# Kernel optimization log

Hardware: AMD Instinct MI355X
Metric: run time of the kernel (lower is better)

Reference implementation:

```python
import jax, jax.numpy as jnp
import numpy as np

B, CDD, HIS, S, D, NH, FF, V, K = 8, 5, 50, 64, 768, 12, 3072, 30522, 8


def _ln(x):
    mu = x.mean(-1, keepdims=True)
    var = ((x - mu) ** 2).mean(-1, keepdims=True)
    return (x - mu) / jnp.sqrt(var + 1e-12)


def _transformer(x, mask, Wq, Wk, Wv, Wo, W1, W2):
    # x: [..., S, D]; mask: [..., S] (float, >0 means valid)
    lead = x.shape[:-2]
    s, d = x.shape[-2], x.shape[-1]
    dh = d // NH
    x2 = x.reshape(-1, s, d)
    m = mask.reshape(-1, s)
    split = lambda t: t.reshape(-1, s, NH, dh).transpose(0, 2, 1, 3)
    q, k, v = split(x2 @ Wq), split(x2 @ Wk), split(x2 @ Wv)
    logits = jnp.einsum('nhqd,nhkd->nhqk', q, k) / jnp.sqrt(jnp.float32(dh))
    logits = logits + jnp.where(m > 0, 0.0, -1e9)[:, None, None, :]
    a = jax.nn.softmax(logits, axis=-1)
    o = jnp.einsum('nhqk,nhkd->nhqd', a, v).transpose(0, 2, 1, 3).reshape(-1, s, d) @ Wo
    h = _ln(x2 + o)
    h = _ln(h + jax.nn.gelu(h @ W1) @ W2)
    h = h.reshape(*lead, s, d)
    return h, h[..., 0, :]


def _build_prefix(subword_index, mask):
    # subword_index: [B, n, S, 2] int; mask: [B, n, 1] float
    b, n = subword_index.shape[0], subword_index.shape[1]
    flat = subword_index[..., 0] * S + subword_index[..., 1]  # [B, n, S]
    dest = jnp.zeros((b * n, S * S), jnp.float32)
    dest = dest.at[jnp.arange(b * n)[:, None], flat.reshape(b * n, S)].set(1.0)
    dest = dest * mask.reshape(b * n, 1)
    prefix = dest.reshape(b, n, S, S)
    # granularity == 'avg' -> L1 normalize rows
    prefix = prefix / jnp.maximum(prefix.sum(-1, keepdims=True), 1e-12)
    return prefix


def setup_inputs() -> dict:
    key = jax.random.key(0)
    ks = jax.random.split(key, 24)
    w = lambda k, shp: jax.random.normal(k, shp, jnp.float32) * 0.02
    inp = {
        'cdd_subword_index': jax.random.randint(ks[0], (B, CDD, S, 2), 0, S, jnp.int32),
        'his_subword_index': jax.random.randint(ks[1], (B, HIS, S, 2), 0, S, jnp.int32),
        'cdd_encoded_index': jax.random.randint(ks[2], (B, CDD, S), 0, V, jnp.int32),
        'his_encoded_index': jax.random.randint(ks[3], (B, HIS, S), 0, V, jnp.int32),
        'cdd_mask': jnp.ones((B, CDD, 1), jnp.float32),
        'his_mask': jnp.ones((B, HIS, 1), jnp.float32),
        'cdd_attn_mask': jnp.ones((B, CDD, S), jnp.float32),
        'his_attn_mask': jnp.ones((B, HIS, S), jnp.float32),
        'emb': w(ks[4], (V, D)),
        'bert_Wq': w(ks[5], (D, D)), 'bert_Wk': w(ks[6], (D, D)),
        'bert_Wv': w(ks[7], (D, D)), 'bert_Wo': w(ks[8], (D, D)),
        'bert_W1': w(ks[9], (D, FF)), 'bert_W2': w(ks[10], (FF, D)),
        'encN_Wq': w(ks[11], (D, D)), 'encN_Wk': w(ks[12], (D, D)),
        'encN_Wv': w(ks[13], (D, D)), 'encN_Wo': w(ks[14], (D, D)),
        'encN_W1': w(ks[15], (D, FF)), 'encN_W2': w(ks[16], (FF, D)),
        'qU': w(ks[17], (D,)),
        'proj_W': w(ks[18], (D, D)), 'proj_b': jnp.zeros((D,), jnp.float32),
    }
    return inp


def reference(cdd_subword_index, his_subword_index, cdd_encoded_index, his_encoded_index,
              cdd_mask, his_mask, cdd_attn_mask, his_attn_mask, emb,
              bert_Wq, bert_Wk, bert_Wv, bert_Wo, bert_W1, bert_W2,
              encN_Wq, encN_Wk, encN_Wv, encN_Wo, encN_W1, encN_W2,
              qU, proj_W, proj_b):
    rt_d = jnp.sqrt(jnp.float32(D))
    # scatter-built one-hot subword->token prefix matrices
    cdd_prefix = _build_prefix(cdd_subword_index, cdd_mask)   # [B,C,S,S]
    his_prefix = _build_prefix(his_subword_index, his_mask)   # [B,H,S,S]
    # pooled attention masks: prefix @ mask
    cdd_attn = jnp.einsum('bcst,bct->bcs', cdd_prefix, cdd_attn_mask)
    his_attn = jnp.einsum('bnst,bnt->bns', his_prefix, his_attn_mask)
    # embedding lookup + subword->token pooling
    cdd_emb = jnp.einsum('bcst,bctd->bcsd', cdd_prefix, emb[cdd_encoded_index])
    his_emb = jnp.einsum('bnst,bntd->bnsd', his_prefix, emb[his_encoded_index])
    # candidate news: BERT encode, take CLS, project
    _, cdd_cls = _transformer(cdd_emb, cdd_attn, bert_Wq, bert_Wk, bert_Wv, bert_Wo, bert_W1, bert_W2)
    cdd_repr = jnp.tanh(cdd_cls @ proj_W + proj_b)            # [B,C,D]
    # history news encoder
    his_hidden, his_cls = _transformer(his_emb, his_attn, encN_Wq, encN_Wk, encN_Wv, encN_Wo, encN_W1, encN_W2)
    # user encoder: attention pooling over history news reprs
    wgt = jax.nn.softmax(jnp.einsum('bnd,d->bn', his_cls, qU) / rt_d, axis=-1)
    user0 = jnp.einsum('bn,bnd->bd', wgt, his_cls)            # [B,D]
    # matching reducer: top-k personalized terms per history news
    scores = jnp.einsum('bnsd,bd->bns', his_hidden, user0) / rt_d
    scores = jnp.where(his_attn > 0, scores, -1e9)
    _, kid = jax.lax.top_k(scores, K)                         # [B,H,K]
    ps_terms = jnp.take_along_axis(his_hidden, kid[..., None], axis=2).reshape(B, HIS * K, D)
    ps_mask = jnp.take_along_axis(his_attn, kid, axis=2).reshape(B, HIS * K)
    # user BERT over selected terms
    _, user_cls = _transformer(ps_terms, ps_mask, bert_Wq, bert_Wk, bert_Wv, bert_Wo, bert_W1, bert_W2)
    user_repr = jnp.tanh(user_cls @ proj_W + proj_b)          # [B,D]
    score = jnp.einsum('bcd,bd->bc', cdd_repr, user_repr) / rt_d
    prob = jax.nn.log_softmax(score, axis=1)
    return prob, kid
```

## Files before the change

kernel.cpp:

```cpp
#include <hip/hip_runtime.h>
#include <math.h>

#define DIM 768
#define NHEAD 12
#define DHEAD 64
#define FFDIM 3072

typedef _Float16 v8h __attribute__((ext_vector_type(8)));
typedef float v4f __attribute__((ext_vector_type(4)));

__device__ __forceinline__ float gelu_f(float x) {
    float x3 = x * x * x;
    return 0.5f * x * (1.0f + tanhf(0.7978845608028654f * (x + 0.044715f * x3)));
}

__device__ __forceinline__ void gl_lds16(const _Float16* g, _Float16* l) {
    __builtin_amdgcn_global_load_lds(
        (const __attribute__((address_space(1))) unsigned int*)(g),
        (__attribute__((address_space(3))) unsigned int*)(l),
        16, 0, 0);
}

struct GemmP {
    const _Float16* A1; const _Float16* A2;
    const _Float16* B1[3]; const _Float16* B2[3];
    float* C[3];
    _Float16* G1; _Float16* G2;
};

__global__ __launch_bounds__(256) void gemm_mfma(GemmP p, int M, int N, int K,
                                                 int nt, int epi, float cdiv, float gscale)
{
    __shared__ _Float16 sm[4][128 * 32];
    const int z = blockIdx.z;
    const int tid = threadIdx.x;
    const int w = tid >> 6, lane = tid & 63;
    const int lm = lane & 15, kg = lane >> 4;
    const int row0 = blockIdx.y << 7, col0 = blockIdx.x << 7;
    const int wm = (w >> 1) << 6, wn = (w & 1) << 6;
    const int rl = (w << 4) + (lane >> 2);
    const int cofs = (lane & 3) << 3;
    const _Float16* A1 = p.A1 + (size_t)row0 * K;
    const _Float16* A2 = p.A2 + (size_t)row0 * K;
    const _Float16* B1 = p.B1[z] + (size_t)col0 * K;
    const _Float16* B2 = p.B2[z] + (size_t)col0 * K;
    _Float16* sA1 = sm[0]; _Float16* sA2 = sm[1];
    _Float16* sB1 = sm[2]; _Float16* sB2 = sm[3];
    const int ldsLo = w * 512, ldsHi = (w + 4) * 512;

    v4f acc[4][4];
#pragma unroll
    for (int i = 0; i < 4; i++)
#pragma unroll
        for (int j = 0; j < 4; j++) acc[i][j] = (v4f){0.f, 0.f, 0.f, 0.f};

    for (int k0 = 0; k0 < K; k0 += 32) {
        __syncthreads();
        size_t glo = (size_t)rl * K + k0 + cofs;
        size_t ghi = glo + (size_t)64 * K;
        gl_lds16(A1 + glo, sA1 + ldsLo); gl_lds16(A1 + ghi, sA1 + ldsHi);
        gl_lds16(B1 + glo, sB1 + ldsLo); gl_lds16(B1 + ghi, sB1 + ldsHi);
        if (nt == 3) {
            gl_lds16(A2 + glo, sA2 + ldsLo); gl_lds16(A2 + ghi, sA2 + ldsHi);
            gl_lds16(B2 + glo, sB2 + ldsLo); gl_lds16(B2 + ghi, sB2 + ldsHi);
        }
        __syncthreads();
        v8h a1[4], b1f[4];
#pragma unroll
        for (int i = 0; i < 4; i++) {
            a1[i]  = *(const v8h*)(sA1 + (wm + (i << 4) + lm) * 32 + (kg << 3));
            b1f[i] = *(const v8h*)(sB1 + (wn + (i << 4) + lm) * 32 + (kg << 3));
        }
        if (nt == 3) {
            v8h a2[4], b2f[4];
#pragma unroll
            for (int i = 0; i < 4; i++) {
                a2[i]  = *(const v8h*)(sA2 + (wm + (i << 4) + lm) * 32 + (kg << 3));
                b2f[i] = *(const v8h*)(sB2 + (wn + (i << 4) + lm) * 32 + (kg << 3));
            }
#pragma unroll
            for (int i = 0; i < 4; i++)
#pragma unroll
                for (int j = 0; j < 4; j++) {
                    acc[i][j] = __builtin_amdgcn_mfma_f32_16x16x32_f16(a1[i], b1f[j], acc[i][j], 0, 0, 0);
                    acc[i][j] = __builtin_amdgcn_mfma_f32_16x16x32_f16(a1[i], b2f[j], acc[i][j], 0, 0, 0);
                    acc[i][j] = __builtin_amdgcn_mfma_f32_16x16x32_f16(a2[i], b1f[j], acc[i][j], 0, 0, 0);
                }
        } else {
#pragma unroll
            for (int i = 0; i < 4; i++)
#pragma unroll
                for (int j = 0; j < 4; j++)
                    acc[i][j] = __builtin_amdgcn_mfma_f32_16x16x32_f16(a1[i], b1f[j], acc[i][j], 0, 0, 0);
        }
    }
    float* C = p.C[z];
#pragma unroll
    for (int i = 0; i < 4; i++) {
        int rb = row0 + wm + (i << 4) + (kg << 2);
#pragma unroll
        for (int j = 0; j < 4; j++) {
            int cc = col0 + wn + (j << 4) + lm;
#pragma unroll
            for (int r = 0; r < 4; r++) {
                float c = acc[i][j][r] * cdiv;
                size_t idx = (size_t)(rb + r) * N + cc;
                if (epi == 0) {
                    C[idx] = c;
                } else {
                    float gv = gelu_f(c) * gscale;
                    _Float16 g1 = (_Float16)gv;
                    p.G1[idx] = g1;
                    p.G2[idx] = (_Float16)(gv - (float)g1);
                }
            }
        }
    }
}

__global__ __launch_bounds__(256) void split2_kernel(const float* __restrict__ X,
    _Float16* __restrict__ A1, _Float16* __restrict__ A2, float s, int n)
{
    int i = (blockIdx.x * 256 + threadIdx.x) * 4;
    if (i >= n) return;
    float4 x = *(const float4*)(X + i);
    float v[4] = {x.x, x.y, x.z, x.w};
#pragma unroll
    for (int u = 0; u < 4; u++) {
        float xs = v[u] * s;
        _Float16 a = (_Float16)xs;
        A1[i + u] = a;
        A2[i + u] = (_Float16)(xs - (float)a);
    }
}

__global__ __launch_bounds__(256) void wsplit_kernel(const float* __restrict__ W,
    _Float16* __restrict__ B1, _Float16* __restrict__ B2, int Kd, int N)
{
    int id = blockIdx.x * 256 + threadIdx.x;
    if (id >= Kd * N) return;
    int n = id / Kd, k = id - n * Kd;
    float v = W[(size_t)k * N + n] * 64.f;
    _Float16 b1 = (_Float16)v;
    B1[id] = b1;
    if (B2) B2[id] = (_Float16)(v - (float)b1);
}

__global__ __launch_bounds__(256) void build_prefix_kernel(const int* __restrict__ sub,
    const float* __restrict__ mask, const float* __restrict__ amask,
    float* __restrict__ P, float* __restrict__ attn_out, int seq0)
{
    __shared__ float pref[64 * 64];
    int gl = blockIdx.x;
    int g = seq0 + gl;
    int tid = threadIdx.x;
    for (int t = tid; t < 4096; t += 256) pref[t] = 0.f;
    __syncthreads();
    if (tid < 64) {
        int r = sub[((size_t)g * 64 + tid) * 2 + 0];
        int c = sub[((size_t)g * 64 + tid) * 2 + 1];
        pref[(r << 6) + c] = 1.0f;
    }
    __syncthreads();
    float m = mask[g];
    int lane = tid & 63, w = tid >> 6;
    for (int s = (w << 4); s < (w << 4) + 16; s++) {
        float v = pref[(s << 6) + lane] * m;
        float rs = v;
#pragma unroll
        for (int o = 32; o; o >>= 1) rs += __shfl_down(rs, o);
        rs = __shfl(rs, 0);
        float nv = v / fmaxf(rs, 1e-12f);
        P[(((size_t)gl << 6) + s) * 64 + lane] = nv;
        float av = nv * amask[((size_t)g << 6) + lane];
#pragma unroll
        for (int o = 32; o; o >>= 1) av += __shfl_down(av, o);
        if (lane == 0) attn_out[((size_t)g << 6) + s] = av;
    }
}

__global__ __launch_bounds__(256) void emb_pool_kernel(const float* __restrict__ P,
    const int* __restrict__ enc, const float* __restrict__ emb,
    float* __restrict__ X, int seq0)
{
    int s = blockIdx.x & 63;
    int gl = blockIdx.x >> 6;
    int g = seq0 + gl;
    int tid = threadIdx.x;
    __shared__ float pw[64];
    __shared__ int tk[64];
    if (tid < 64) {
        pw[tid] = P[(((size_t)gl << 6) + s) * 64 + tid];
        tk[tid] = enc[((size_t)g << 6) + tid];
    }
    __syncthreads();
    float a0 = 0.f, a1 = 0.f, a2 = 0.f;
    for (int t = 0; t < 64; t++) {
        float w = pw[t];
        if (w != 0.f) {
            const float* er = emb + (size_t)tk[t] * DIM;
            a0 = fmaf(w, er[tid], a0);
            a1 = fmaf(w, er[tid + 256], a1);
            a2 = fmaf(w, er[tid + 512], a2);
        }
    }
    size_t ro = (((size_t)gl << 6) + s) * DIM;
    X[ro + tid] = a0; X[ro + tid + 256] = a1; X[ro + tid + 512] = a2;
}

__global__ __launch_bounds__(256) void attn_fused64(const float* __restrict__ Q,
    const float* __restrict__ Km, const float* __restrict__ V,
    const float* __restrict__ mask, _Float16* __restrict__ o1, _Float16* __restrict__ o2)
{
    __shared__ float Ks[64 * 65];
    __shared__ float Vs[64 * 65];
    __shared__ float Qs[64 * 65];
    int h = blockIdx.x % NHEAD;
    int g = blockIdx.x / NHEAD;
    int tid = threadIdx.x, lane = tid & 63, w = tid >> 6;
    {
        int r = tid >> 2, c0 = (tid & 3) << 4;
        const float* qp = Q  + ((size_t)g * 64 + r) * DIM + h * DHEAD + c0;
        const float* kp = Km + ((size_t)g * 64 + r) * DIM + h * DHEAD + c0;
        const float* vp = V  + ((size_t)g * 64 + r) * DIM + h * DHEAD + c0;
#pragma unroll
        for (int u = 0; u < 16; u += 4) {
            float4 qv = *(const float4*)(qp + u);
            float4 kv = *(const float4*)(kp + u);
            float4 vv = *(const float4*)(vp + u);
            int o = r * 65 + c0 + u;
            Qs[o+0]=qv.x; Qs[o+1]=qv.y; Qs[o+2]=qv.z; Qs[o+3]=qv.w;
            Ks[o+0]=kv.x; Ks[o+1]=kv.y; Ks[o+2]=kv.z; Ks[o+3]=kv.w;
            Vs[o+0]=vv.x; Vs[o+1]=vv.y; Vs[o+2]=vv.z; Vs[o+3]=vv.w;
        }
    }
    __syncthreads();
    float mk = mask[(size_t)g * 64 + lane] > 0.f ? 0.f : -1e9f;
    for (int il = 0; il < 16; il++) {
        int i = (w << 4) + il;
        float d = 0.f;
        for (int t = 0; t < 64; t++) d = fmaf(Qs[i * 65 + t], Ks[lane * 65 + t], d);
        float l = d * 0.125f + mk;
        float mx = l;
#pragma unroll
        for (int o = 32; o; o >>= 1) mx = fmaxf(mx, __shfl_xor(mx, o));
        float e = expf(l - mx);
        float s = e;
#pragma unroll
        for (int o = 32; o; o >>= 1) s += __shfl_xor(s, o);
        float p = e / s;
        float acc = 0.f;
        for (int j = 0; j < 64; j++) {
            float pj = __shfl(p, j);
            acc = fmaf(pj, Vs[j * 65 + lane], acc);
        }
        size_t ob = ((size_t)g * 64 + i) * DIM + h * DHEAD + lane;
        float os = acc * 64.f;
        _Float16 h1 = (_Float16)os;
        o1[ob] = h1;
        o2[ob] = (_Float16)(os - (float)h1);
    }
}

#define SSTR 449
__global__ __launch_bounds__(256) void attn_flash400(const float* __restrict__ Q,
    const float* __restrict__ Km, const float* __restrict__ V,
    const float* __restrict__ mask, _Float16* __restrict__ o1, _Float16* __restrict__ o2)
{
    __shared__ _Float16 Kt[64 * 64];
    __shared__ float Sc[16 * SSTR];
    int qt = blockIdx.x % 25;
    int h  = (blockIdx.x / 25) % NHEAD;
    int g  = blockIdx.x / (25 * NHEAD);
    int tid = threadIdx.x, w = tid >> 6, lane = tid & 63, lm = lane & 15, kg = lane >> 4;

    v8h aq0, aq1;
    {
        const float* qp = Q + ((size_t)(g * 400 + qt * 16 + lm)) * DIM + h * DHEAD;
#pragma unroll
        for (int u = 0; u < 8; u++) {
            aq0[u] = (_Float16)qp[kg * 8 + u];
            aq1[u] = (_Float16)qp[32 + kg * 8 + u];
        }
    }
    for (int jt = 0; jt < 7; jt++) {
        int j0 = jt * 64;
        __syncthreads();
        {
            int jr = tid >> 2, c0 = (tid & 3) << 4;
            int j = j0 + jr;
            _Float16* kd = Kt + jr * 64 + c0;
            if (j < 400) {
                const float* kp = Km + ((size_t)(g * 400 + j)) * DIM + h * DHEAD + c0;
#pragma unroll
                for (int u = 0; u < 16; u++) kd[u] = (_Float16)kp[u];
            } else {
#pragma unroll
                for (int u = 0; u < 16; u++) kd[u] = (_Float16)0.f;
            }
        }
        __syncthreads();
        v8h b0, b1;
#pragma unroll
        for (int u = 0; u < 8; u++) {
            b0[u] = Kt[(w * 16 + lm) * 64 + kg * 8 + u];
            b1[u] = Kt[(w * 16 + lm) * 64 + 32 + kg * 8 + u];
        }
        v4f c = {0.f, 0.f, 0.f, 0.f};
        c = __builtin_amdgcn_mfma_f32_16x16x32_f16(aq0, b0, c, 0, 0, 0);
        c = __builtin_amdgcn_mfma_f32_16x16x32_f16(aq1, b1, c, 0, 0, 0);
        int jj = j0 + w * 16 + lm;
        float mv = (jj < 400) ? (mask[g * 400 + jj] > 0.f ? 0.f : -1e9f) : -1e9f;
#pragma unroll
        for (int r = 0; r < 4; r++)
            Sc[(kg * 4 + r) * SSTR + jj] = c[r] * 0.125f + mv;
    }
    __syncthreads();
    for (int rr = 0; rr < 4; rr++) {
        int r = w * 4 + rr;
        float mx = -INFINITY;
#pragma unroll
        for (int c7 = 0; c7 < 7; c7++) mx = fmaxf(mx, Sc[r * SSTR + c7 * 64 + lane]);
#pragma unroll
        for (int o = 32; o; o >>= 1) mx = fmaxf(mx, __shfl_xor(mx, o));
        float s = 0.f;
        float ev[7];
#pragma unroll
        for (int c7 = 0; c7 < 7; c7++) { ev[c7] = expf(Sc[r * SSTR + c7 * 64 + lane] - mx); s += ev[c7]; }
#pragma unroll
        for (int o = 32; o; o >>= 1) s += __shfl_xor(s, o);
        float inv = 1.f / s;
#pragma unroll
        for (int c7 = 0; c7 < 7; c7++) Sc[r * SSTR + c7 * 64 + lane] = ev[c7] * inv;
    }
    __syncthreads();
    v4f o = {0.f, 0.f, 0.f, 0.f};
    for (int kc = 0; kc < 14; kc++) {
        v8h a, b;
#pragma unroll
        for (int u = 0; u < 8; u++) a[u] = (_Float16)Sc[lm * SSTR + kc * 32 + kg * 8 + u];
#pragma unroll
        for (int u = 0; u < 8; u++) {
            int j = kc * 32 + kg * 8 + u;
            b[u] = (j < 400) ? (_Float16)V[((size_t)(g * 400 + j)) * DIM + h * DHEAD + w * 16 + lm]
                             : (_Float16)0.f;
        }
        o = __builtin_amdgcn_mfma_f32_16x16x32_f16(a, b, o, 0, 0, 0);
    }
#pragma unroll
    for (int r = 0; r < 4; r++) {
        int qr = qt * 16 + kg * 4 + r;
        size_t ob = ((size_t)(g * 400 + qr)) * DIM + h * DHEAD + w * 16 + lm;
        float os = o[r] * 64.f;
        _Float16 h1 = (_Float16)os;
        o1[ob] = h1; o2[ob] = (_Float16)(os - (float)h1);
    }
}

__global__ __launch_bounds__(256) void add_ln_kernel(const float* __restrict__ X,
    const float* __restrict__ Y, float* __restrict__ Out)
{
    int r = blockIdx.x, tid = threadIdx.x;
    size_t base = (size_t)r * DIM;
    float v0 = X[base + tid] + Y[base + tid];
    float v1 = X[base + tid + 256] + Y[base + tid + 256];
    float v2 = X[base + tid + 512] + Y[base + tid + 512];
    __shared__ float red[256];
    red[tid] = v0 + v1 + v2; __syncthreads();
    for (int o = 128; o; o >>= 1) { if (tid < o) red[tid] += red[tid + o]; __syncthreads(); }
    float mu = red[0] * (1.f / 768.f);
    __syncthreads();
    float d0 = v0 - mu, d1 = v1 - mu, d2 = v2 - mu;
    red[tid] = d0 * d0 + d1 * d1 + d2 * d2; __syncthreads();
    for (int o = 128; o; o >>= 1) { if (tid < o) red[tid] += red[tid + o]; __syncthreads(); }
    float rstd = rsqrtf(red[0] * (1.f / 768.f) + 1e-12f);
    Out[base + tid] = d0 * rstd;
    Out[base + tid + 256] = d1 * rstd;
    Out[base + tid + 512] = d2 * rstd;
}

__global__ void cls_copy_kernel(const float* __restrict__ H, float* __restrict__ cls, int S) {
    int g = blockIdx.x, tid = threadIdx.x;
    size_t src = (size_t)g * S * DIM;
    cls[(size_t)g * DIM + tid]       = H[src + tid];
    cls[(size_t)g * DIM + tid + 256] = H[src + tid + 256];
    cls[(size_t)g * DIM + tid + 512] = H[src + tid + 512];
}

__global__ __launch_bounds__(256) void gemm_kernel(const float* __restrict__ A,
    const float* __restrict__ B, float* __restrict__ C,
    int M, int N, int Kd, int epi, const float* __restrict__ bias)
{
    __shared__ float As[16][64];
    __shared__ float Bs[16][64];
    int tid = threadIdx.x;
    int tx = tid & 15, ty = tid >> 4;
    int row0 = blockIdx.y << 6, col0 = blockIdx.x << 6;
    int ar = tid >> 2, ak = (tid & 3) << 2;
    int bc = tid & 63, bk0 = tid >> 6;
    const float* Ap = A + (size_t)(row0 + ar) * Kd + ak;
    const float* Bp = B + (size_t)bk0 * N + col0 + bc;
    bool aval = (row0 + ar) < M;
    float acc[4][4];
#pragma unroll
    for (int i = 0; i < 4; i++)
#pragma unroll
        for (int j = 0; j < 4; j++) acc[i][j] = 0.f;
    for (int k0 = 0; k0 < Kd; k0 += 16) {
        float4 a4 = make_float4(0.f, 0.f, 0.f, 0.f);
        if (aval) a4 = *(const float4*)(Ap + k0);
        As[ak + 0][ar] = a4.x; As[ak + 1][ar] = a4.y;
        As[ak + 2][ar] = a4.z; As[ak + 3][ar] = a4.w;
#pragma unroll
        for (int i = 0; i < 4; i++)
            Bs[bk0 + 4 * i][bc] = Bp[(size_t)(k0 + 4 * i) * N];
        __syncthreads();
#pragma unroll
        for (int kk = 0; kk < 16; kk++) {
            float4 av = *(const float4*)&As[kk][ty << 2];
            float4 bv = *(const float4*)&Bs[kk][tx << 2];
            float aa[4] = {av.x, av.y, av.z, av.w};
            float bb[4] = {bv.x, bv.y, bv.z, bv.w};
#pragma unroll
            for (int i = 0; i < 4; i++)
#pragma unroll
                for (int j = 0; j < 4; j++)
                    acc[i][j] = fmaf(aa[i], bb[j], acc[i][j]);
        }
        __syncthreads();
    }
#pragma unroll
    for (int i = 0; i < 4; i++) {
        int r = row0 + (ty << 2) + i;
        if (r >= M) continue;
        float v[4];
#pragma unroll
        for (int j = 0; j < 4; j++) {
            float x = acc[i][j];
            if (epi == 1) x = gelu_f(x);
            else if (epi == 2) x = tanhf(x + bias[col0 + (tx << 2) + j]);
            v[j] = x;
        }
        *(float4*)(C + (size_t)r * N + col0 + (tx << 2)) = make_float4(v[0], v[1], v[2], v[3]);
    }
}

__global__ __launch_bounds__(256) void user_pool_kernel(const float* __restrict__ cls,
    const float* __restrict__ qU, float* __restrict__ user0)
{
    int b = blockIdx.x, tid = threadIdx.x;
    __shared__ float red[256];
    __shared__ float wv[64];
    const float scale = 0.03608439182435161f;
    for (int n = 0; n < 50; n++) {
        const float* cr = cls + ((size_t)(b * 50 + n)) * DIM;
        float d = 0.f;
        for (int t = tid; t < DIM; t += 256) d = fmaf(cr[t], qU[t], d);
        red[tid] = d; __syncthreads();
        for (int o = 128; o; o >>= 1) { if (tid < o) red[tid] += red[tid + o]; __syncthreads(); }
        if (tid == 0) wv[n] = red[0] * scale;
        __syncthreads();
    }
    if (tid == 0) {
        float mx = -INFINITY;
        for (int n = 0; n < 50; n++) mx = fmaxf(mx, wv[n]);
        float s = 0.f;
        for (int n = 0; n < 50; n++) { float e = expf(wv[n] - mx); wv[n] = e; s += e; }
        float inv = 1.f / s;
        for (int n = 0; n < 50; n++) wv[n] *= inv;
    }
    __syncthreads();
    for (int d = tid; d < DIM; d += 256) {
        float a = 0.f;
        for (int n = 0; n < 50; n++) a = fmaf(wv[n], cls[((size_t)(b * 50 + n)) * DIM + d], a);
        user0[(size_t)b * DIM + d] = a;
    }
}

__global__ __launch_bounds__(256) void topk_kernel(const float* __restrict__ hid,
    const float* __restrict__ user0, const float* __restrict__ attn,
    float* __restrict__ kid_f, int* __restrict__ kid_i, float* __restrict__ ps_mask)
{
    int bn = blockIdx.x;
    int b = bn / 50;
    int tid = threadIdx.x, lane = tid & 63, w = tid >> 6;
    __shared__ float sc[64];
    const float* u = user0 + (size_t)b * DIM;
    const float scale = 0.03608439182435161f;
    for (int s = w; s < 64; s += 4) {
        const float* hr = hid + ((size_t)bn * 64 + s) * DIM;
        float d = 0.f;
        for (int t = lane; t < DIM; t += 64) d = fmaf(hr[t], u[t], d);
#pragma unroll
        for (int o = 32; o; o >>= 1) d += __shfl_down(d, o);
        if (lane == 0) {
            float a = attn[(size_t)bn * 64 + s];
            sc[s] = (a > 0.f) ? d * scale : -1e9f;
        }
    }
    __syncthreads();
    if (tid == 0) {
        unsigned long long used = 0ull;
        for (int k = 0; k < 8; k++) {
            float best = -INFINITY; int bi = 0;
            for (int s = 0; s < 64; s++) {
                if ((used >> s) & 1ull) continue;
                if (sc[s] > best) { best = sc[s]; bi = s; }
            }
            used |= (1ull << bi);
            kid_i[bn * 8 + k] = bi;
            kid_f[bn * 8 + k] = (float)bi;
            ps_mask[bn * 8 + k] = attn[(size_t)bn * 64 + bi];
        }
    }
}

__global__ void gather_kernel(const float* __restrict__ hid, const int* __restrict__ kid_i,
    float* __restrict__ X)
{
    int r = blockIdx.x, tid = threadIdx.x;
    int s = kid_i[r];
    int bn = r >> 3;
    const float* src = hid + ((size_t)bn * 64 + s) * DIM;
    float* dst = X + (size_t)r * DIM;
    dst[tid] = src[tid];
    dst[tid + 256] = src[tid + 256];
    dst[tid + 512] = src[tid + 512];
}

__global__ __launch_bounds__(256) void final_kernel(const float* __restrict__ cdd_repr,
    const float* __restrict__ user_repr, float* __restrict__ out)
{
    int b = blockIdx.x, tid = threadIdx.x;
    __shared__ float red[256];
    __shared__ float sc[5];
    const float scale = 0.03608439182435161f;
    for (int c = 0; c < 5; c++) {
        const float* cr = cdd_repr + ((size_t)(b * 5 + c)) * DIM;
        const float* ur = user_repr + (size_t)b * DIM;
        float d = 0.f;
        for (int t = tid; t < DIM; t += 256) d = fmaf(cr[t], ur[t], d);
        red[tid] = d; __syncthreads();
        for (int o = 128; o; o >>= 1) { if (tid < o) red[tid] += red[tid + o]; __syncthreads(); }
        if (tid == 0) sc[c] = red[0] * scale;
        __syncthreads();
    }
    if (tid == 0) {
        float mx = -INFINITY;
        for (int c = 0; c < 5; c++) mx = fmaxf(mx, sc[c]);
        float s = 0.f;
        for (int c = 0; c < 5; c++) s += expf(sc[c] - mx);
        float lse = logf(s) + mx;
        for (int c = 0; c < 5; c++) out[b * 5 + c] = sc[c] - lse;
    }
}

extern "C" void kernel_launch(void* const* d_in, const int* in_sizes, int n_in,
                              void* d_out, int out_size, void* d_ws, size_t ws_size,
                              hipStream_t stream)
{
    (void)in_sizes; (void)n_in; (void)out_size;
    const int*   cdd_sub   = (const int*)d_in[0];
    const int*   his_sub   = (const int*)d_in[1];
    const int*   cdd_enc   = (const int*)d_in[2];
    const int*   his_enc   = (const int*)d_in[3];
    const float* cdd_mask  = (const float*)d_in[4];
    const float* his_mask  = (const float*)d_in[5];
    const float* cdd_amask = (const float*)d_in[6];
    const float* his_amask = (const float*)d_in[7];
    const float* emb = (const float*)d_in[8];
    const float* bWsrc[6] = {(const float*)d_in[9],  (const float*)d_in[10], (const float*)d_in[11],
                             (const float*)d_in[12], (const float*)d_in[13], (const float*)d_in[14]};
    const float* eWsrc[6] = {(const float*)d_in[15], (const float*)d_in[16], (const float*)d_in[17],
                             (const float*)d_in[18], (const float*)d_in[19], (const float*)d_in[20]};
    const float* qU = (const float*)d_in[21];
    const float* pW = (const float*)d_in[22];
    const float* pb = (const float*)d_in[23];
    float* out = (float*)d_out;

    const size_t FIXED = 124ull * 1000 * 1000;
    int CH = 50;
    {
        int opts[4] = {400, 200, 100, 50};
        for (int i = 0; i < 4; i++) {
            size_t need = FIXED + (size_t)opts[i] * 64 * 21760;
            if (need <= ws_size) { CH = opts[i]; break; }
        }
    }
    const size_t RC = (size_t)CH * 64;

    char* wsb = (char*)d_ws;
    size_t off = 0;
    auto allocB = [&](size_t bytes) { char* p = wsb + off; off += (bytes + 255) & ~(size_t)255; return p; };
    float* R_X = (float*)allocB(RC * 768 * 4);
    float* R_Q = (float*)allocB(RC * 768 * 4);
    float* R_K = (float*)allocB(RC * 768 * 4);
    float* R_V = (float*)allocB(RC * 768 * 4);
    _Float16* s1h = (_Float16*)allocB(RC * 768 * 2);
    _Float16* s2h = (_Float16*)allocB(RC * 768 * 2);
    _Float16* g2h = (_Float16*)allocB(RC * 3072 * 2);
    float* R_Pa = (float*)allocB((size_t)CH * 4096 * 4);
    float* hisH  = (float*)allocB((size_t)400 * 64 * 768 * 4);
    float* hisC  = (float*)allocB((size_t)400 * 768 * 4);
    float* cddC  = (float*)allocB((size_t)40 * 768 * 4);
    float* userC = (float*)allocB((size_t)8 * 768 * 4);
    float* hisA  = (float*)allocB((size_t)400 * 64 * 4);
    float* cddA  = (float*)allocB((size_t)40 * 64 * 4);
    float* cddR  = (float*)allocB((size_t)40 * 768 * 4);
    float* userR = (float*)allocB((size_t)8 * 768 * 4);
    float* user0 = (float*)allocB((size_t)8 * 768 * 4);
    float* psM   = (float*)allocB((size_t)8 * 400 * 4);
    int*   kidI  = (int*)allocB(3200 * 4);
    size_t wsz[6] = {589824, 589824, 589824, 589824, 2359296, 2359296};
    _Float16 *eB1[6], *eB2[6], *bB1[6];
    for (int i = 0; i < 6; i++) eB1[i] = (_Float16*)allocB(wsz[i] * 2);
    for (int i = 0; i < 6; i++) eB2[i] = (_Float16*)allocB(wsz[i] * 2);
    for (int i = 0; i < 6; i++) bB1[i] = (_Float16*)allocB(wsz[i] * 2);
    _Float16* g1h = (_Float16*)R_K;

    int wk[6] = {768, 768, 768, 768, 768, 3072};
    int wn[6] = {768, 768, 768, 768, 3072, 768};
    for (int i = 0; i < 6; i++) {
        int n = wk[i] * wn[i];
        wsplit_kernel<<<(n + 255) / 256, 256, 0, stream>>>(eWsrc[i], eB1[i], eB2[i], wk[i], wn[i]);
        wsplit_kernel<<<(n + 255) / 256, 256, 0, stream>>>(bWsrc[i], bB1[i], nullptr, wk[i], wn[i]);
    }

    auto tf = [&](const float* maskp, int nseq, int S, _Float16* const* B1, _Float16* const* B2,
                  int nt, float* outH, float* clsD) {
        int R = nseq * S, MB = R >> 7;
        int nsplit = (R * 768 / 4 + 255) / 256;
        split2_kernel<<<nsplit, 256, 0, stream>>>(R_X, s1h, s2h, 64.f, R * 768);
        GemmP gq{};
        gq.A1 = s1h; gq.A2 = s2h;
        for (int z = 0; z < 3; z++) { gq.B1[z] = B1[z]; gq.B2[z] = B2 ? B2[z] : B1[z]; }
        gq.C[0] = R_Q; gq.C[1] = R_K; gq.C[2] = R_V;
        gemm_mfma<<<dim3(6, MB, 3), 256, 0, stream>>>(gq, R, 768, 768, nt, 0, 1.f / 4096.f, 0.f);
        if (S == 64) {
            attn_fused64<<<nseq * NHEAD, 256, 0, stream>>>(R_Q, R_K, R_V, maskp, s1h, s2h);
        } else {
            attn_flash400<<<8 * NHEAD * 25, 256, 0, stream>>>(R_Q, R_K, R_V, maskp, s1h, s2h);
        }
        GemmP go{};
        go.A1 = s1h; go.A2 = s2h;
        go.B1[0] = B1[3]; go.B2[0] = B2 ? B2[3] : B1[3];
        go.C[0] = R_Q;
        gemm_mfma<<<dim3(6, MB, 1), 256, 0, stream>>>(go, R, 768, 768, nt, 0, 1.f / 4096.f, 0.f);
        add_ln_kernel<<<R, 256, 0, stream>>>(R_X, R_Q, R_X);
        split2_kernel<<<nsplit, 256, 0, stream>>>(R_X, s1h, s2h, 1.f, R * 768);
        GemmP g1{};
        g1.A1 = s1h; g1.A2 = s2h;
        g1.B1[0] = B1[4]; g1.B2[0] = B2 ? B2[4] : B1[4];
        g1.G1 = g1h; g1.G2 = g2h; g1.C[0] = nullptr;
        gemm_mfma<<<dim3(24, MB, 1), 256, 0, stream>>>(g1, R, 3072, 768, nt, 1, 1.f / 64.f, 16.f);
        GemmP g2{};
        g2.A1 = g1h; g2.A2 = g2h;
        g2.B1[0] = B1[5]; g2.B2[0] = B2 ? B2[5] : B1[5];
        g2.C[0] = R_Q;
        gemm_mfma<<<dim3(6, MB, 1), 256, 0, stream>>>(g2, R, 768, 3072, nt, 0, 1.f / 1024.f, 0.f);
        add_ln_kernel<<<R, 256, 0, stream>>>(R_X, R_Q, outH);
        cls_copy_kernel<<<nseq, 256, 0, stream>>>(outH, clsD, S);
    };

    build_prefix_kernel<<<40, 256, 0, stream>>>(cdd_sub, cdd_mask, cdd_amask, R_Pa, cddA, 0);
    emb_pool_kernel<<<40 * 64, 256, 0, stream>>>(R_Pa, cdd_enc, emb, R_X, 0);
    tf(cddA, 40, 64, bB1, nullptr, 1, R_X, cddC);
    gemm_kernel<<<dim3(12, 1), 256, 0, stream>>>(cddC, pW, cddR, 40, 768, 768, 2, pb);

    for (int seq0 = 0; seq0 < 400; seq0 += CH) {
        build_prefix_kernel<<<CH, 256, 0, stream>>>(his_sub, his_mask, his_amask, R_Pa, hisA, seq0);
        emb_pool_kernel<<<CH * 64, 256, 0, stream>>>(R_Pa, his_enc, emb, R_X, seq0);
        tf(hisA + (size_t)seq0 * 64, CH, 64, eB1, eB2, 3,
           hisH + (size_t)seq0 * 64 * DIM, hisC + (size_t)seq0 * DIM);
    }

    user_pool_kernel<<<8, 256, 0, stream>>>(hisC, qU, user0);
    topk_kernel<<<400, 256, 0, stream>>>(hisH, user0, hisA, out + 40, kidI, psM);
    gather_kernel<<<3200, 256, 0, stream>>>(hisH, kidI, R_X);

    tf(psM, 8, 400, bB1, nullptr, 1, R_X, userC);
    gemm_kernel<<<dim3(12, 1), 256, 0, stream>>>(userC, pW, userR, 8, 768, 768, 2, pb);

    final_kernel<<<8, 256, 0, stream>>>(cddR, userR, out);
}
```

Before: 3.629 ms.

## Batch candidate and history encoders, fuse splits into producers, tile weight transpose

```diff
diff --git a/kernel.cpp b/kernel.cpp
--- a/kernel.cpp
+++ b/kernel.cpp
@@ -23,13 +23,14 @@
 
 struct GemmP {
     const _Float16* A1; const _Float16* A2;
-    const _Float16* B1[3]; const _Float16* B2[3];
+    const _Float16* eB1[3]; const _Float16* eB2[3]; const _Float16* bB1[3];
     float* C[3];
     _Float16* G1; _Float16* G2;
+    int bnd;
 };
 
 __global__ __launch_bounds__(256) void gemm_mfma(GemmP p, int M, int N, int K,
-                                                 int nt, int epi, float cdiv, float gscale)
+                                                 int epi, float cdiv, float gscale)
 {
     __shared__ _Float16 sm[4][128 * 32];
     const int z = blockIdx.z;
@@ -40,10 +41,13 @@
     const int wm = (w >> 1) << 6, wn = (w & 1) << 6;
     const int rl = (w << 4) + (lane >> 2);
     const int cofs = (lane & 3) << 3;
+    int nt; const _Float16 *B1p, *B2p;
+    if (row0 < p.bnd) { nt = 3; B1p = p.eB1[z]; B2p = p.eB2[z]; }
+    else             { nt = 1; B1p = p.bB1[z]; B2p = p.bB1[z]; }
     const _Float16* A1 = p.A1 + (size_t)row0 * K;
     const _Float16* A2 = p.A2 + (size_t)row0 * K;
-    const _Float16* B1 = p.B1[z] + (size_t)col0 * K;
-    const _Float16* B2 = p.B2[z] + (size_t)col0 * K;
+    const _Float16* B1 = B1p + (size_t)col0 * K;
+    const _Float16* B2 = B2p + (size_t)col0 * K;
     _Float16* sA1 = sm[0]; _Float16* sA2 = sm[1];
     _Float16* sB1 = sm[2]; _Float16* sB2 = sm[3];
     const int ldsLo = w * 512, ldsHi = (w + 4) * 512;
@@ -118,51 +122,64 @@
     }
 }
 
-__global__ __launch_bounds__(256) void split2_kernel(const float* __restrict__ X,
-    _Float16* __restrict__ A1, _Float16* __restrict__ A2, float s, int n)
-{
-    int i = (blockIdx.x * 256 + threadIdx.x) * 4;
-    if (i >= n) return;
-    float4 x = *(const float4*)(X + i);
-    float v[4] = {x.x, x.y, x.z, x.w};
-#pragma unroll
-    for (int u = 0; u < 4; u++) {
-        float xs = v[u] * s;
-        _Float16 a = (_Float16)xs;
-        A1[i + u] = a;
-        A2[i + u] = (_Float16)(xs - (float)a);
-    }
-}
-
-__global__ __launch_bounds__(256) void wsplit_kernel(const float* __restrict__ W,
-    _Float16* __restrict__ B1, _Float16* __restrict__ B2, int Kd, int N)
-{
-    int id = blockIdx.x * 256 + threadIdx.x;
-    if (id >= Kd * N) return;
-    int n = id / Kd, k = id - n * Kd;
-    float v = W[(size_t)k * N + n] * 64.f;
-    _Float16 b1 = (_Float16)v;
-    B1[id] = b1;
-    if (B2) B2[id] = (_Float16)(v - (float)b1);
-}
-
-__global__ __launch_bounds__(256) void build_prefix_kernel(const int* __restrict__ sub,
-    const float* __restrict__ mask, const float* __restrict__ amask,
-    float* __restrict__ P, float* __restrict__ attn_out, int seq0)
+struct WJobs {
+    const float* src[12];
+    _Float16* d1[12]; _Float16* d2[12];
+    int K[12]; int N[12]; int start[12];
+};
+__global__ __launch_bounds__(256) void wsplit_tr(WJobs jb)
+{
+    __shared__ float sh[32 * 33];
+    int bid = blockIdx.x;
+    int ji = 0;
+#pragma unroll
+    for (int i = 1; i < 12; i++) if (bid >= jb.start[i]) ji = i;
+    const float* src = jb.src[ji];
+    _Float16* d1 = jb.d1[ji]; _Float16* d2 = jb.d2[ji];
+    int K = jb.K[ji], N = jb.N[ji];
+    int t = bid - jb.start[ji];
+    int tilesN = N >> 5;
+    int tk = t / tilesN, tn = t - tk * tilesN;
+    int k0 = tk << 5, n0 = tn << 5;
+    int c = threadIdx.x & 31, rr = threadIdx.x >> 5;
+#pragma unroll
+    for (int pph = 0; pph < 4; pph++) {
+        int r = rr + (pph << 3);
+        sh[c * 33 + r] = src[(size_t)(k0 + r) * N + n0 + c];
+    }
+    __syncthreads();
+#pragma unroll
+    for (int pph = 0; pph < 4; pph++) {
+        int rn = rr + (pph << 3);
+        float v = sh[rn * 33 + c] * 64.f;
+        _Float16 b1 = (_Float16)v;
+        size_t idx = (size_t)(n0 + rn) * K + k0 + c;
+        d1[idx] = b1;
+        if (d2) d2[idx] = (_Float16)(v - (float)b1);
+    }
+}
+
+__global__ __launch_bounds__(256) void build_prefix2(const int* __restrict__ hisSub,
+    const float* __restrict__ hisMask, const float* __restrict__ hisAmask,
+    const int* __restrict__ cddSub, const float* __restrict__ cddMask,
+    const float* __restrict__ cddAmask,
+    float* __restrict__ P, float* __restrict__ hisA, float* __restrict__ cddA)
 {
     __shared__ float pref[64 * 64];
-    int gl = blockIdx.x;
-    int g = seq0 + gl;
+    int g = blockIdx.x;
+    const int* sub; const float* mask; const float* amask; float* aout; int li;
+    if (g < 400) { sub = hisSub; mask = hisMask; amask = hisAmask; aout = hisA; li = g; }
+    else         { sub = cddSub; mask = cddMask; amask = cddAmask; aout = cddA; li = g - 400; }
     int tid = threadIdx.x;
     for (int t = tid; t < 4096; t += 256) pref[t] = 0.f;
     __syncthreads();
     if (tid < 64) {
-        int r = sub[((size_t)g * 64 + tid) * 2 + 0];
-        int c = sub[((size_t)g * 64 + tid) * 2 + 1];
+        int r = sub[((size_t)li * 64 + tid) * 2 + 0];
+        int c = sub[((size_t)li * 64 + tid) * 2 + 1];
         pref[(r << 6) + c] = 1.0f;
     }
     __syncthreads();
-    float m = mask[g];
+    float m = mask[li];
     int lane = tid & 63, w = tid >> 6;
     for (int s = (w << 4); s < (w << 4) + 16; s++) {
         float v = pref[(s << 6) + lane] * m;
@@ -171,52 +188,74 @@
         for (int o = 32; o; o >>= 1) rs += __shfl_down(rs, o);
         rs = __shfl(rs, 0);
         float nv = v / fmaxf(rs, 1e-12f);
-        P[(((size_t)gl << 6) + s) * 64 + lane] = nv;
-        float av = nv * amask[((size_t)g << 6) + lane];
+        P[(((size_t)g << 6) + s) * 64 + lane] = nv;
+        float av = nv * amask[((size_t)li << 6) + lane];
 #pragma unroll
         for (int o = 32; o; o >>= 1) av += __shfl_down(av, o);
-        if (lane == 0) attn_out[((size_t)g << 6) + s] = av;
-    }
-}
-
-__global__ __launch_bounds__(256) void emb_pool_kernel(const float* __restrict__ P,
-    const int* __restrict__ enc, const float* __restrict__ emb,
-    float* __restrict__ X, int seq0)
-{
-    int s = blockIdx.x & 63;
-    int gl = blockIdx.x >> 6;
-    int g = seq0 + gl;
+        if (lane == 0) aout[((size_t)li << 6) + s] = av;
+    }
+}
+
+__global__ __launch_bounds__(256) void emb_pool2(const float* __restrict__ P,
+    const int* __restrict__ encHis, const int* __restrict__ encCdd,
+    const float* __restrict__ emb, float* __restrict__ X,
+    _Float16* __restrict__ s1, _Float16* __restrict__ s2, int gOffHis, int gMid)
+{
+    int gl = blockIdx.x >> 2, q = blockIdx.x & 3;
+    int g; const int* enc;
+    if (gl < gMid) { g = gOffHis + gl; enc = encHis + (size_t)g * 64; }
+    else { int gc = gl - gMid; g = 400 + gc; enc = encCdd + (size_t)gc * 64; }
     int tid = threadIdx.x;
-    __shared__ float pw[64];
+    __shared__ float pw[16][64];
     __shared__ int tk[64];
-    if (tid < 64) {
-        pw[tid] = P[(((size_t)gl << 6) + s) * 64 + tid];
-        tk[tid] = enc[((size_t)g << 6) + tid];
-    }
-    __syncthreads();
-    float a0 = 0.f, a1 = 0.f, a2 = 0.f;
+    if (tid < 64) tk[tid] = enc[tid];
+    for (int u = tid; u < 1024; u += 256) {
+        int si = u >> 6, t = u & 63;
+        pw[si][t] = P[((size_t)g * 64 + q * 16 + si) * 64 + t];
+    }
+    __syncthreads();
+    float acc[16][3];
+#pragma unroll
+    for (int si = 0; si < 16; si++) { acc[si][0] = 0.f; acc[si][1] = 0.f; acc[si][2] = 0.f; }
     for (int t = 0; t < 64; t++) {
-        float w = pw[t];
-        if (w != 0.f) {
-            const float* er = emb + (size_t)tk[t] * DIM;
-            a0 = fmaf(w, er[tid], a0);
-            a1 = fmaf(w, er[tid + 256], a1);
-            a2 = fmaf(w, er[tid + 512], a2);
-        }
-    }
-    size_t ro = (((size_t)gl << 6) + s) * DIM;
-    X[ro + tid] = a0; X[ro + tid + 256] = a1; X[ro + tid + 512] = a2;
+        const float* er = emb + (size_t)tk[t] * DIM;
+        float e0 = er[tid], e1 = er[tid + 256], e2 = er[tid + 512];
+#pragma unroll
+        for (int si = 0; si < 16; si++) {
+            float w = pw[si][t];
+            acc[si][0] = fmaf(w, e0, acc[si][0]);
+            acc[si][1] = fmaf(w, e1, acc[si][1]);
+            acc[si][2] = fmaf(w, e2, acc[si][2]);
+        }
+    }
+#pragma unroll
+    for (int si = 0; si < 16; si++) {
+        size_t base = ((size_t)gl * 64 + q * 16 + si) * DIM;
+#pragma unroll
+        for (int cci = 0; cci < 3; cci++) {
+            int cc = tid + (cci << 8);
+            float v = acc[si][cci];
+            X[base + cc] = v;
+            float xs = v * 64.f;
+            _Float16 a = (_Float16)xs;
+            s1[base + cc] = a;
+            s2[base + cc] = (_Float16)(xs - (float)a);
+        }
+    }
 }
 
 __global__ __launch_bounds__(256) void attn_fused64(const float* __restrict__ Q,
     const float* __restrict__ Km, const float* __restrict__ V,
-    const float* __restrict__ mask, _Float16* __restrict__ o1, _Float16* __restrict__ o2)
+    const float* __restrict__ maskHis, const float* __restrict__ maskCdd, int gMid,
+    _Float16* __restrict__ o1, _Float16* __restrict__ o2)
 {
     __shared__ float Ks[64 * 65];
     __shared__ float Vs[64 * 65];
     __shared__ float Qs[64 * 65];
     int h = blockIdx.x % NHEAD;
     int g = blockIdx.x / NHEAD;
+    const float* mrow = (g < gMid) ? maskHis + (size_t)g * 64
+                                   : maskCdd + (size_t)(g - gMid) * 64;
     int tid = threadIdx.x, lane = tid & 63, w = tid >> 6;
     {
         int r = tid >> 2, c0 = (tid & 3) << 4;
@@ -235,7 +274,7 @@
         }
     }
     __syncthreads();
-    float mk = mask[(size_t)g * 64 + lane] > 0.f ? 0.f : -1e9f;
+    float mk = mrow[lane] > 0.f ? 0.f : -1e9f;
     for (int il = 0; il < 16; il++) {
         int i = (w << 4) + il;
         float d = 0.f;
@@ -357,8 +396,10 @@
     }
 }
 
-__global__ __launch_bounds__(256) void add_ln_kernel(const float* __restrict__ X,
-    const float* __restrict__ Y, float* __restrict__ Out)
+__global__ __launch_bounds__(256) void add_ln2(const float* __restrict__ X,
+    const float* __restrict__ Y, float* __restrict__ outA, float* __restrict__ outB,
+    int bndRow, _Float16* __restrict__ S1, _Float16* __restrict__ S2, float ss,
+    float* __restrict__ cls, int clsOffA, int clsOffB, int S)
 {
     int r = blockIdx.x, tid = threadIdx.x;
     size_t base = (size_t)r * DIM;
@@ -374,17 +415,21 @@
     red[tid] = d0 * d0 + d1 * d1 + d2 * d2; __syncthreads();
     for (int o = 128; o; o >>= 1) { if (tid < o) red[tid] += red[tid + o]; __syncthreads(); }
     float rstd = rsqrtf(red[0] * (1.f / 768.f) + 1e-12f);
-    Out[base + tid] = d0 * rstd;
-    Out[base + tid + 256] = d1 * rstd;
-    Out[base + tid + 512] = d2 * rstd;
-}
-
-__global__ void cls_copy_kernel(const float* __restrict__ H, float* __restrict__ cls, int S) {
-    int g = blockIdx.x, tid = threadIdx.x;
-    size_t src = (size_t)g * S * DIM;
-    cls[(size_t)g * DIM + tid]       = H[src + tid];
-    cls[(size_t)g * DIM + tid + 256] = H[src + tid + 256];
-    cls[(size_t)g * DIM + tid + 512] = H[src + tid + 512];
+    float o0 = d0 * rstd, o1 = d1 * rstd, o2 = d2 * rstd;
+    float* Out = (r < bndRow) ? outA + base : outB + (size_t)(r - bndRow) * DIM;
+    Out[tid] = o0; Out[tid + 256] = o1; Out[tid + 512] = o2;
+    if (S1) {
+        float x0 = o0 * ss, x1 = o1 * ss, x2 = o2 * ss;
+        _Float16 a0 = (_Float16)x0, a1 = (_Float16)x1, a2 = (_Float16)x2;
+        S1[base + tid] = a0;        S2[base + tid] = (_Float16)(x0 - (float)a0);
+        S1[base + tid + 256] = a1;  S2[base + tid + 256] = (_Float16)(x1 - (float)a1);
+        S1[base + tid + 512] = a2;  S2[base + tid + 512] = (_Float16)(x2 - (float)a2);
+    }
+    if (cls && (r % S) == 0) {
+        int g = (r < bndRow) ? clsOffA + r / S : clsOffB + (r - bndRow) / S;
+        float* cd = cls + (size_t)g * DIM;
+        cd[tid] = o0; cd[tid + 256] = o1; cd[tid + 512] = o2;
+    }
 }
 
 __global__ __launch_bounds__(256) void gemm_kernel(const float* __restrict__ A,
@@ -515,17 +560,24 @@
     }
 }
 
-__global__ void gather_kernel(const float* __restrict__ hid, const int* __restrict__ kid_i,
-    float* __restrict__ X)
+__global__ void gather2(const float* __restrict__ hid, const int* __restrict__ kid_i,
+    float* __restrict__ X, _Float16* __restrict__ s1, _Float16* __restrict__ s2)
 {
     int r = blockIdx.x, tid = threadIdx.x;
     int s = kid_i[r];
     int bn = r >> 3;
     const float* src = hid + ((size_t)bn * 64 + s) * DIM;
-    float* dst = X + (size_t)r * DIM;
-    dst[tid] = src[tid];
-    dst[tid + 256] = src[tid + 256];
-    dst[tid + 512] = src[tid + 512];
+    size_t base = (size_t)r * DIM;
+#pragma unroll
+    for (int cci = 0; cci < 3; cci++) {
+        int cc = tid + (cci << 8);
+        float v = src[cc];
+        X[base + cc] = v;
+        float xs = v * 64.f;
+        _Float16 a = (_Float16)xs;
+        s1[base + cc] = a;
+        s2[base + cc] = (_Float16)(xs - (float)a);
+    }
 }
 
 __global__ __launch_bounds__(256) void final_kernel(const float* __restrict__ cdd_repr,
@@ -578,20 +630,30 @@
     const float* pb = (const float*)d_in[23];
     float* out = (float*)d_out;
 
-    const size_t FIXED = 124ull * 1000 * 1000;
-    int CH = 50;
-    {
-        int opts[4] = {400, 200, 100, 50};
-        for (int i = 0; i < 4; i++) {
-            size_t need = FIXED + (size_t)opts[i] * 64 * 21760;
-            if (need <= ws_size) { CH = opts[i]; break; }
-        }
-    }
-    const size_t RC = (size_t)CH * 64;
+    auto al256 = [](size_t b) { return (b + 255) & ~(size_t)255; };
+    auto needBytes = [&](size_t RCx) -> size_t {
+        size_t t = 0;
+        t += 4 * al256(RCx * 768 * 4);
+        t += 2 * al256(RCx * 768 * 2);
+        t += al256(RCx * 3072 * 2);
+        t += al256((size_t)440 * 4096 * 4);
+        t += al256((size_t)400 * 64 * 768 * 4);
+        t += al256((size_t)448 * 768 * 4);
+        t += 8 * al256(131072);
+        t += 3 * (4 * al256((size_t)589824 * 2) + 2 * al256((size_t)2359296 * 2));
+        return t;
+    };
+    const int NSopts[9] = {400, 200, 134, 100, 66, 50, 34, 24, 10};
+    int NS = 10;
+    for (int i = 0; i < 9; i++) {
+        size_t RCt = (size_t)NSopts[i] * 64 + 2560;
+        if (needBytes(RCt) <= ws_size) { NS = NSopts[i]; break; }
+    }
+    const size_t RC = (size_t)NS * 64 + 2560;
 
     char* wsb = (char*)d_ws;
     size_t off = 0;
-    auto allocB = [&](size_t bytes) { char* p = wsb + off; off += (bytes + 255) & ~(size_t)255; return p; };
+    auto allocB = [&](size_t bytes) { char* p = wsb + off; off += al256(bytes); return p; };
     float* R_X = (float*)allocB(RC * 768 * 4);
     float* R_Q = (float*)allocB(RC * 768 * 4);
     float* R_K = (float*)allocB(RC * 768 * 4);
@@ -599,86 +661,104 @@
     _Float16* s1h = (_Float16*)allocB(RC * 768 * 2);
     _Float16* s2h = (_Float16*)allocB(RC * 768 * 2);
     _Float16* g2h = (_Float16*)allocB(RC * 3072 * 2);
-    float* R_Pa = (float*)allocB((size_t)CH * 4096 * 4);
-    float* hisH  = (float*)allocB((size_t)400 * 64 * 768 * 4);
-    float* hisC  = (float*)allocB((size_t)400 * 768 * 4);
-    float* cddC  = (float*)allocB((size_t)40 * 768 * 4);
-    float* userC = (float*)allocB((size_t)8 * 768 * 4);
-    float* hisA  = (float*)allocB((size_t)400 * 64 * 4);
-    float* cddA  = (float*)allocB((size_t)40 * 64 * 4);
-    float* cddR  = (float*)allocB((size_t)40 * 768 * 4);
-    float* userR = (float*)allocB((size_t)8 * 768 * 4);
-    float* user0 = (float*)allocB((size_t)8 * 768 * 4);
-    float* psM   = (float*)allocB((size_t)8 * 400 * 4);
-    int*   kidI  = (int*)allocB(3200 * 4);
+    float* Pa   = (float*)allocB((size_t)440 * 4096 * 4);
+    float* hisH = (float*)allocB((size_t)400 * 64 * 768 * 4);
+    float* cls  = (float*)allocB((size_t)448 * 768 * 4);
+    float* userC = (float*)allocB(131072);
+    float* hisA  = (float*)allocB(131072);
+    float* cddA  = (float*)allocB(131072);
+    float* cddR  = (float*)allocB(131072);
+    float* userR = (float*)allocB(131072);
+    float* user0 = (float*)allocB(131072);
+    float* psM   = (float*)allocB(131072);
+    int*   kidI  = (int*)allocB(131072);
     size_t wsz[6] = {589824, 589824, 589824, 589824, 2359296, 2359296};
-    _Float16 *eB1[6], *eB2[6], *bB1[6];
-    for (int i = 0; i < 6; i++) eB1[i] = (_Float16*)allocB(wsz[i] * 2);
-    for (int i = 0; i < 6; i++) eB2[i] = (_Float16*)allocB(wsz[i] * 2);
-    for (int i = 0; i < 6; i++) bB1[i] = (_Float16*)allocB(wsz[i] * 2);
+    _Float16 *eB1s[6], *eB2s[6], *bB1s[6];
+    for (int i = 0; i < 6; i++) eB1s[i] = (_Float16*)allocB(wsz[i] * 2);
+    for (int i = 0; i < 6; i++) eB2s[i] = (_Float16*)allocB(wsz[i] * 2);
+    for (int i = 0; i < 6; i++) bB1s[i] = (_Float16*)allocB(wsz[i] * 2);
     _Float16* g1h = (_Float16*)R_K;
+    float* cddTrash = (float*)g2h;
 
     int wk[6] = {768, 768, 768, 768, 768, 3072};
     int wn[6] = {768, 768, 768, 768, 3072, 768};
-    for (int i = 0; i < 6; i++) {
-        int n = wk[i] * wn[i];
-        wsplit_kernel<<<(n + 255) / 256, 256, 0, stream>>>(eWsrc[i], eB1[i], eB2[i], wk[i], wn[i]);
-        wsplit_kernel<<<(n + 255) / 256, 256, 0, stream>>>(bWsrc[i], bB1[i], nullptr, wk[i], wn[i]);
-    }
-
-    auto tf = [&](const float* maskp, int nseq, int S, _Float16* const* B1, _Float16* const* B2,
-                  int nt, float* outH, float* clsD) {
-        int R = nseq * S, MB = R >> 7;
-        int nsplit = (R * 768 / 4 + 255) / 256;
-        split2_kernel<<<nsplit, 256, 0, stream>>>(R_X, s1h, s2h, 64.f, R * 768);
-        GemmP gq{};
-        gq.A1 = s1h; gq.A2 = s2h;
-        for (int z = 0; z < 3; z++) { gq.B1[z] = B1[z]; gq.B2[z] = B2 ? B2[z] : B1[z]; }
+    {
+        WJobs jb{};
+        int st = 0;
+        for (int i = 0; i < 6; i++) {
+            jb.src[i] = eWsrc[i]; jb.d1[i] = eB1s[i]; jb.d2[i] = eB2s[i];
+            jb.K[i] = wk[i]; jb.N[i] = wn[i]; jb.start[i] = st;
+            st += (wk[i] >> 5) * (wn[i] >> 5);
+        }
+        for (int i = 0; i < 6; i++) {
+            jb.src[6 + i] = bWsrc[i]; jb.d1[6 + i] = bB1s[i]; jb.d2[6 + i] = nullptr;
+            jb.K[6 + i] = wk[i]; jb.N[6 + i] = wn[i]; jb.start[6 + i] = st;
+            st += (wk[i] >> 5) * (wn[i] >> 5);
+        }
+        wsplit_tr<<<st, 256, 0, stream>>>(jb);
+    }
+
+    build_prefix2<<<440, 256, 0, stream>>>(his_sub, his_mask, his_amask,
+                                           cdd_sub, cdd_mask, cdd_amask, Pa, hisA, cddA);
+
+    auto mkP = [&](int sl, int bnd) {
+        GemmP g{};
+        g.A1 = s1h; g.A2 = s2h;
+        for (int z = 0; z < 3; z++) {
+            g.eB1[z] = eB1s[sl]; g.eB2[z] = eB2s[sl]; g.bB1[z] = bB1s[sl];
+        }
+        g.bnd = bnd;
+        return g;
+    };
+
+    auto tf = [&](int M, int bnd, int nseqTot, int gMid, const float* mHis,
+                  float* outA, float* outB, float* clsArena, int clsOffA, int clsOffB,
+                  int S, bool userAttn) {
+        int MB = M >> 7;
+        GemmP gq = mkP(0, bnd);
+        for (int z = 0; z < 3; z++) { gq.eB1[z] = eB1s[z]; gq.eB2[z] = eB2s[z]; gq.bB1[z] = bB1s[z]; }
         gq.C[0] = R_Q; gq.C[1] = R_K; gq.C[2] = R_V;
-        gemm_mfma<<<dim3(6, MB, 3), 256, 0, stream>>>(gq, R, 768, 768, nt, 0, 1.f / 4096.f, 0.f);
-        if (S == 64) {
-            attn_fused64<<<nseq * NHEAD, 256, 0, stream>>>(R_Q, R_K, R_V, maskp, s1h, s2h);
+        gemm_mfma<<<dim3(6, MB, 3), 256, 0, stream>>>(gq, M, 768, 768, 0, 1.f / 4096.f, 0.f);
+        if (!userAttn) {
+            attn_fused64<<<nseqTot * NHEAD, 256, 0, stream>>>(R_Q, R_K, R_V, mHis, cddA, gMid, s1h, s2h);
         } else {
-            attn_flash400<<<8 * NHEAD * 25, 256, 0, stream>>>(R_Q, R_K, R_V, maskp, s1h, s2h);
-        }
-        GemmP go{};
-        go.A1 = s1h; go.A2 = s2h;
-        go.B1[0] = B1[3]; go.B2[0] = B2 ? B2[3] : B1[3];
+            attn_flash400<<<8 * NHEAD * 25, 256, 0, stream>>>(R_Q, R_K, R_V, mHis, s1h, s2h);
+        }
+        GemmP go = mkP(3, bnd);
         go.C[0] = R_Q;
-        gemm_mfma<<<dim3(6, MB, 1), 256, 0, stream>>>(go, R, 768, 768, nt, 0, 1.f / 4096.f, 0.f);
-        add_ln_kernel<<<R, 256, 0, stream>>>(R_X, R_Q, R_X);
-        split2_kernel<<<nsplit, 256, 0, stream>>>(R_X, s1h, s2h, 1.f, R * 768);
-        GemmP g1{};
-        g1.A1 = s1h; g1.A2 = s2h;
-        g1.B1[0] = B1[4]; g1.B2[0] = B2 ? B2[4] : B1[4];
-        g1.G1 = g1h; g1.G2 = g2h; g1.C[0] = nullptr;
-        gemm_mfma<<<dim3(24, MB, 1), 256, 0, stream>>>(g1, R, 3072, 768, nt, 1, 1.f / 64.f, 16.f);
-        GemmP g2{};
-        g2.A1 = g1h; g2.A2 = g2h;
-        g2.B1[0] = B1[5]; g2.B2[0] = B2 ? B2[5] : B1[5];
-        g2.C[0] = R_Q;
-        gemm_mfma<<<dim3(6, MB, 1), 256, 0, stream>>>(g2, R, 768, 3072, nt, 0, 1.f / 1024.f, 0.f);
-        add_ln_kernel<<<R, 256, 0, stream>>>(R_X, R_Q, outH);
-        cls_copy_kernel<<<nseq, 256, 0, stream>>>(outH, clsD, S);
+        gemm_mfma<<<dim3(6, MB, 1), 256, 0, stream>>>(go, M, 768, 768, 0, 1.f / 4096.f, 0.f);
+        add_ln2<<<M, 256, 0, stream>>>(R_X, R_Q, R_X, R_X, M, s1h, s2h, 1.f, nullptr, 0, 0, 64);
+        GemmP g1 = mkP(4, bnd);
+        g1.G1 = g1h; g1.G2 = g2h;
+        gemm_mfma<<<dim3(24, MB, 1), 256, 0, stream>>>(g1, M, 3072, 768, 1, 1.f / 64.f, 16.f);
+        GemmP g2 = mkP(5, bnd);
+        g2.A1 = g1h; g2.A2 = g2h; g2.C[0] = R_Q;
+        gemm_mfma<<<dim3(6, MB, 1), 256, 0, stream>>>(g2, M, 768, 3072, 0, 1.f / 1024.f, 0.f);
+        add_ln2<<<M, 256, 0, stream>>>(R_X, R_Q, outA, outB, bnd, nullptr, nullptr, 0.f,
+                                       clsArena, clsOffA, clsOffB, S);
     };
 
-    build_prefix_kernel<<<40, 256, 0, stream>>>(cdd_sub, cdd_mask, cdd_amask, R_Pa, cddA, 0);
-    emb_pool_kernel<<<40 * 64, 256, 0, stream>>>(R_Pa, cdd_enc, emb, R_X, 0);
-    tf(cddA, 40, 64, bB1, nullptr, 1, R_X, cddC);
-    gemm_kernel<<<dim3(12, 1), 256, 0, stream>>>(cddC, pW, cddR, 40, 768, 768, 2, pb);
-
-    for (int seq0 = 0; seq0 < 400; seq0 += CH) {
-        build_prefix_kernel<<<CH, 256, 0, stream>>>(his_sub, his_mask, his_amask, R_Pa, hisA, seq0);
-        emb_pool_kernel<<<CH * 64, 256, 0, stream>>>(R_Pa, his_enc, emb, R_X, seq0);
-        tf(hisA + (size_t)seq0 * 64, CH, 64, eB1, eB2, 3,
-           hisH + (size_t)seq0 * 64 * DIM, hisC + (size_t)seq0 * DIM);
-    }
-
-    user_pool_kernel<<<8, 256, 0, stream>>>(hisC, qU, user0);
+    int done = 0;
+    bool first = true;
+    while (done < 400) {
+        int ns = NS < (400 - done) ? NS : (400 - done);
+        int hisRows = ns * 64;
+        int M = hisRows + (first ? 2560 : 0);
+        int nseqTot = ns + (first ? 40 : 0);
+        emb_pool2<<<nseqTot * 4, 256, 0, stream>>>(Pa, his_enc, cdd_enc, emb, R_X, s1h, s2h, done, ns);
+        tf(M, hisRows, nseqTot, ns, hisA + (size_t)done * 64,
+           hisH + (size_t)done * 64 * DIM, cddTrash, cls, done, 400, 64, false);
+        done += ns;
+        first = false;
+    }
+
+    gemm_kernel<<<dim3(12, 1), 256, 0, stream>>>(cls + (size_t)400 * 768, pW, cddR, 40, 768, 768, 2, pb);
+
+    user_pool_kernel<<<8, 256, 0, stream>>>(cls, qU, user0);
     topk_kernel<<<400, 256, 0, stream>>>(hisH, user0, hisA, out + 40, kidI, psM);
-    gather_kernel<<<3200, 256, 0, stream>>>(hisH, kidI, R_X);
-
-    tf(psM, 8, 400, bB1, nullptr, 1, R_X, userC);
+    gather2<<<3200, 256, 0, stream>>>(hisH, kidI, R_X, s1h, s2h);
+
+    tf(3200, 0, 8, 0, psM, hisH, hisH, userC, 0, 0, 400, true);
     gemm_kernel<<<dim3(12, 1), 256, 0, stream>>>(userC, pW, userR, 8, 768, 768, 2, pb);
 
     final_kernel<<<8, 256, 0, stream>>>(cddR, userR, out);
```

Measured after the change: 3.216 ms. -11.4%, faster.
